# Performance work log

Hardware: AMD Instinct MI355X
Metric: run time of the kernel (lower is better)

Reference implementation:

```python
import jax, jax.numpy as jnp
import numpy as np

ALPHA = 1.0

def setup_inputs() -> dict:
    key = jax.random.key(0)
    k1, k2 = jax.random.split(key)
    x = jax.random.normal(k1, (65536, 512), dtype=jnp.float32)
    clusters = jax.random.normal(k2, (256, 512), dtype=jnp.float32)
    return {"x": x, "clusters": clusters}

def reference(x, clusters):
    # Squared Euclidean distance to each centroid via the GEMM expansion
    x2 = jnp.sum(x * x, axis=1, keepdims=True)            # (B, 1)
    c2 = jnp.sum(clusters * clusters, axis=1)             # (K,)
    cross = x @ clusters.T                                # (B, K) GEMM
    d2 = jnp.maximum(x2 + c2 - 2.0 * cross, 0.0)          # (B, K)
    # Student-t kernel (DEC soft assignment)
    q = 1.0 / (1.0 + d2 / ALPHA)
    q = q ** ((ALPHA + 1.0) / 2.0)
    q = q / jnp.sum(q, axis=1, keepdims=True)             # row-normalize
    return q
```

## Files before the change

### kernel.cpp

```cpp
#include <hip/hip_runtime.h>
#include <hip/hip_bf16.h>


typedef __attribute__((ext_vector_type(4))) short short4v;
typedef __attribute__((ext_vector_type(8))) short short8v;
typedef __attribute__((ext_vector_type(4))) float f32x4;

#define DDIM 512
#define KCL  256
#define BM   64
#define NT   512
#define NTILES 16
#define BTILE  8192

__device__ __forceinline__ short f2bf(float f) {
    __hip_bfloat16 h = __float2bfloat16(f);
    return __builtin_bit_cast(short, h);
}

__device__ __forceinline__ void glds16(const void* g, void* l) {
    __builtin_amdgcn_global_load_lds(
        (const __attribute__((address_space(1))) unsigned int*)g,
        (__attribute__((address_space(3))) unsigned int*)l, 16, 0, 0);
}

__global__ void prep(const float* __restrict__ cl, short* __restrict__ wsB,
                     float* __restrict__ wsC2) {
    const int t = threadIdx.x;
    if (blockIdx.x < 64) {
        const int u = blockIdx.x * 256 + t;
        const int img = u >> 10, gi = u & 1023;
        const int g = gi >> 6, lq = (gi >> 4) & 3, l15 = gi & 15;
        const float* src = cl + (size_t)(g * 16 + l15) * DDIM + img * 32 + lq * 8;
        float4 a = *(const float4*)src;
        float4 b = *(const float4*)(src + 4);
        short8v s;
        s[0]=f2bf(a.x); s[1]=f2bf(a.y); s[2]=f2bf(a.z); s[3]=f2bf(a.w);
        s[4]=f2bf(b.x); s[5]=f2bf(b.y); s[6]=f2bf(b.z); s[7]=f2bf(b.w);
        *(short8v*)&wsB[(size_t)u * 8] = s;
    } else {
        const int cidx = (blockIdx.x - 64) * 16 + (t >> 4);
        const int j = t & 15;
        const float* src = cl + (size_t)cidx * DDIM + j * 32;
        float s = 0.f;
#pragma unroll
        for (int i = 0; i < 8; ++i) {
            float4 v = ((const float4*)src)[i];
            s += v.x*v.x + v.y*v.y + v.z*v.z + v.w*v.w;
        }
        s += __shfl_xor(s, 1); s += __shfl_xor(s, 2);
        s += __shfl_xor(s, 4); s += __shfl_xor(s, 8);
        if (j == 0) wsC2[cidx] = s;
    }
}

#define SFENCE() __builtin_amdgcn_sched_barrier(0)
#define BARV1() asm volatile("s_waitcnt vmcnt(1) lgkmcnt(0)\ns_barrier" ::: "memory")
#define BARV0() asm volatile("s_waitcnt vmcnt(0) lgkmcnt(0)\ns_barrier" ::: "memory")
#define BARV2() asm volatile("s_waitcnt vmcnt(2) lgkmcnt(0)\ns_barrier" ::: "memory")

__global__ __launch_bounds__(NT, 4)
void dec_main(const float* __restrict__ x, const short* __restrict__ wsB,
              const float* __restrict__ wsC2, float* __restrict__ out) {
    __shared__ __align__(16) short lA[2][2048];
    __shared__ __align__(16) short lB[2][8192];
    __shared__ float s_x2[BM];
    __shared__ float s_rs[4][BM];

    const int t = threadIdx.x, lane = t & 63, w = t >> 6;
    const int rg = w >> 2, cg = w & 3;
    const int l15 = lane & 15, lq = lane >> 4;
    const int row0 = blockIdx.x * BM;

    const int srow = t >> 3;
    const int sk4  = (t & 7) << 2;
    const float* xs = x + (size_t)(row0 + srow) * DDIM + sk4;
    const int awr = (srow >> 4) * 512 + (srow & 15) * 32
                  + ((t & 7) >> 1) * 8 + ((t & 7) & 1) * 4;

    f32x4 acc[2][4];
#pragma unroll
    for (int m = 0; m < 2; ++m)
#pragma unroll
        for (int n = 0; n < 4; ++n) acc[m][n] = (f32x4){0.f,0.f,0.f,0.f};
    float x2p = 0.f;
    float4 X0, X1, X2;

#define GLDS(TT, LBN)                                        \
    {  const short* src_ = wsB + (size_t)(TT) * BTILE;       \
       glds16(src_ + t * 8,        (LBN) + t * 8);           \
       glds16(src_ + 4096 + t * 8, (LBN) + 4096 + t * 8); }

#define LOADX(TT, XR)  { XR = *(const float4*)(xs + (TT) * 32); }

#define CVT(XR, LAN)                                                             \
    {  short4v s_;                                                               \
       s_[0]=f2bf(XR.x); s_[1]=f2bf(XR.y); s_[2]=f2bf(XR.z); s_[3]=f2bf(XR.w);   \
       x2p += XR.x*XR.x + XR.y*XR.y + XR.z*XR.z + XR.w*XR.w;                     \
       *(short4v*)&(LAN)[awr] = s_; }

#define MSTEP(LAN, LBN)                                                          \
    {  short8v a0 = *(const short8v*)&(LAN)[rg*1024 + l15*32 + lq*8];            \
       short8v a1 = *(const short8v*)&(LAN)[rg*1024 + 512 + l15*32 + lq*8];      \
       short8v b0 = *(const short8v*)&(LBN)[cg*2048 + lane*8];                   \
       short8v b1 = *(const short8v*)&(LBN)[cg*2048 + 512  + lane*8];            \
       short8v b2 = *(const short8v*)&(LBN)[cg*2048 + 1024 + lane*8];            \
       short8v b3 = *(const short8v*)&(LBN)[cg*2048 + 1536 + lane*8];            \
       acc[0][0] = __builtin_amdgcn_mfma_f32_16x16x32_bf16(a0, b0, acc[0][0], 0,0,0); \
       acc[0][1] = __builtin_amdgcn_mfma_f32_16x16x32_bf16(a0, b1, acc[0][1], 0,0,0); \
       acc[0][2] = __builtin_amdgcn_mfma_f32_16x16x32_bf16(a0, b2, acc[0][2], 0,0,0); \
       acc[0][3] = __builtin_amdgcn_mfma_f32_16x16x32_bf16(a0, b3, acc[0][3], 0,0,0); \
       acc[1][0] = __builtin_amdgcn_mfma_f32_16x16x32_bf16(a1, b0, acc[1][0], 0,0,0); \
       acc[1][1] = __builtin_amdgcn_mfma_f32_16x16x32_bf16(a1, b1, acc[1][1], 0,0,0); \
       acc[1][2] = __builtin_amdgcn_mfma_f32_16x16x32_bf16(a1, b2, acc[1][2], 0,0,0); \
       acc[1][3] = __builtin_amdgcn_mfma_f32_16x16x32_bf16(a1, b3, acc[1][3], 0,0,0); }

#define ITER(J, AC, BC, AN, BN, XC, XL)                                          \
    {  if ((J) + 1 < NTILES) GLDS((J) + 1, BN);                                  \
       SFENCE();                                                                 \
       if ((J) + 1 < NTILES) CVT(XC, AN);                                        \
       MSTEP(AC, BC);                                                            \
       SFENCE();                                                                 \
       if ((J) + 3 < NTILES) { LOADX((J) + 3, XL); }                             \
       SFENCE();                                                                 \
       if ((J) + 1 < NTILES) { if ((J) + 3 < NTILES) BARV1(); else BARV0(); } }

    LOADX(0, X0);
    GLDS(0, lB[0]);
    LOADX(1, X1);
    LOADX(2, X2);
    SFENCE();
    CVT(X0, lA[0]);
    SFENCE();
    BARV2();

    ITER( 0, lA[0], lB[0], lA[1], lB[1], X1, X0)
    ITER( 1, lA[1], lB[1], lA[0], lB[0], X2, X1)
    ITER( 2, lA[0], lB[0], lA[1], lB[1], X0, X2)
    ITER( 3, lA[1], lB[1], lA[0], lB[0], X1, X0)
    ITER( 4, lA[0], lB[0], lA[1], lB[1], X2, X1)
    ITER( 5, lA[1], lB[1], lA[0], lB[0], X0, X2)
    ITER( 6, lA[0], lB[0], lA[1], lB[1], X1, X0)
    ITER( 7, lA[1], lB[1], lA[0], lB[0], X2, X1)
    ITER( 8, lA[0], lB[0], lA[1], lB[1], X0, X2)
    ITER( 9, lA[1], lB[1], lA[0], lB[0], X1, X0)
    ITER(10, lA[0], lB[0], lA[1], lB[1], X2, X1)
    ITER(11, lA[1], lB[1], lA[0], lB[0], X0, X2)
    ITER(12, lA[0], lB[0], lA[1], lB[1], X1, X0)
    ITER(13, lA[1], lB[1], lA[0], lB[0], X2, X1)
    ITER(14, lA[0], lB[0], lA[1], lB[1], X0, X0)
    ITER(15, lA[1], lB[1], lA[0], lB[0], X0, X0)

    x2p += __shfl_xor(x2p, 1); x2p += __shfl_xor(x2p, 2); x2p += __shfl_xor(x2p, 4);
    if ((t & 7) == 0) s_x2[srow] = x2p;
    __syncthreads();

    float c2a[4];
#pragma unroll
    for (int n = 0; n < 4; ++n) c2a[n] = wsC2[cg*64 + n*16 + l15];

#pragma unroll
    for (int m = 0; m < 2; ++m)
#pragma unroll
        for (int n = 0; n < 4; ++n)
#pragma unroll
            for (int r = 0; r < 4; ++r) {
                const int rw = rg*32 + m*16 + lq*4 + r;
                float d2 = fmaxf(s_x2[rw] + c2a[n] - 2.0f * acc[m][n][r], 0.0f);
                acc[m][n][r] = 1.0f / (1.0f + d2);
            }

#pragma unroll
    for (int m = 0; m < 2; ++m)
#pragma unroll
        for (int r = 0; r < 4; ++r) {
            float p = acc[m][0][r] + acc[m][1][r] + acc[m][2][r] + acc[m][3][r];
            p += __shfl_xor(p, 1); p += __shfl_xor(p, 2);
            p += __shfl_xor(p, 4); p += __shfl_xor(p, 8);
            if (l15 == 0) s_rs[cg][rg*32 + m*16 + lq*4 + r] = p;
        }
    __syncthreads();

#pragma unroll
    for (int m = 0; m < 2; ++m)
#pragma unroll
        for (int r = 0; r < 4; ++r) {
            const int rw = rg*32 + m*16 + lq*4 + r;
            const float rinv = 1.0f / (s_rs[0][rw] + s_rs[1][rw] + s_rs[2][rw] + s_rs[3][rw]);
            float* o = out + (size_t)(row0 + rw) * KCL + cg*64 + l15;
#pragma unroll
            for (int n = 0; n < 4; ++n)
                o[n * 16] = acc[m][n][r] * rinv;
        }
}

extern "C" void kernel_launch(void* const* d_in, const int* in_sizes, int n_in,
                              void* d_out, int out_size, void* d_ws, size_t ws_size,
                              hipStream_t stream) {
    const float* x  = (const float*)d_in[0];
    const float* cl = (const float*)d_in[1];
    float* out = (float*)d_out;
    short* wsB  = (short*)d_ws;
    float* wsC2 = (float*)((char*)d_ws + (size_t)NTILES * BTILE * sizeof(short));

    prep<<<80, 256, 0, stream>>>(cl, wsB, wsC2);
    const int B = in_sizes[0] / DDIM;
    dec_main<<<B / BM, NT, 0, stream>>>(x, wsB, wsC2, out);
}
```

Before: 54.07 us.

## Triple-buffer B tiles, single-buffer A with two barriers, raise occupancy

Restructures the K-loop pipeline so centroid tiles sit in a three-slot LDS ring with a prefetch distance of two, while the converted x tile uses one LDS buffer. Each iteration now has two barriers: one after the MFMA reads and one after the next A tile is written. The A layout is rearranged so each lane reads a contiguous 16-byte chunk, the epilogue scratch arrays are aliased onto the A buffer, and launch bounds rise from 4 to 6 blocks per CU. The aim is deeper B prefetch and higher occupancy, at the cost of an extra barrier per iteration and more register pressure.

```diff
diff --git a/kernel.cpp b/kernel.cpp
--- a/kernel.cpp
+++ b/kernel.cpp
@@ -54,18 +54,18 @@
     }
 }
 
-#define SFENCE() __builtin_amdgcn_sched_barrier(0)
-#define BARV1() asm volatile("s_waitcnt vmcnt(1) lgkmcnt(0)\ns_barrier" ::: "memory")
-#define BARV0() asm volatile("s_waitcnt vmcnt(0) lgkmcnt(0)\ns_barrier" ::: "memory")
-#define BARV2() asm volatile("s_waitcnt vmcnt(2) lgkmcnt(0)\ns_barrier" ::: "memory")
-
-__global__ __launch_bounds__(NT, 4)
+#define SFENCE()  __builtin_amdgcn_sched_barrier(0)
+#define BARLGKM() asm volatile("s_waitcnt lgkmcnt(0)\ns_barrier" ::: "memory")
+#define BARV3()   asm volatile("s_waitcnt vmcnt(3) lgkmcnt(0)\ns_barrier" ::: "memory")
+#define BARV0()   asm volatile("s_waitcnt vmcnt(0) lgkmcnt(0)\ns_barrier" ::: "memory")
+
+__global__ __launch_bounds__(NT, 6)
 void dec_main(const float* __restrict__ x, const short* __restrict__ wsB,
               const float* __restrict__ wsC2, float* __restrict__ out) {
-    __shared__ __align__(16) short lA[2][2048];
-    __shared__ __align__(16) short lB[2][8192];
-    __shared__ float s_x2[BM];
-    __shared__ float s_rs[4][BM];
+    __shared__ __align__(16) short lB3[3][BTILE];
+    __shared__ __align__(16) short lA[2048];
+    float* const s_x2 = (float*)lA;
+    float* const s_rs = ((float*)lA) + 64;
 
     const int t = threadIdx.x, lane = t & 63, w = t >> 6;
     const int rg = w >> 2, cg = w & 3;
@@ -73,10 +73,9 @@
     const int row0 = blockIdx.x * BM;
 
     const int srow = t >> 3;
-    const int sk4  = (t & 7) << 2;
-    const float* xs = x + (size_t)(row0 + srow) * DDIM + sk4;
-    const int awr = (srow >> 4) * 512 + (srow & 15) * 32
-                  + ((t & 7) >> 1) * 8 + ((t & 7) & 1) * 4;
+    const float* xs = x + (size_t)(row0 + srow) * DDIM + (t & 7) * 4;
+    const int awr = (srow >> 4) * 512 + ((srow & 15) + 16 * ((t & 7) >> 1)) * 8
+                  + ((t & 7) & 1) * 4;
 
     f32x4 acc[2][4];
 #pragma unroll
@@ -84,7 +83,7 @@
 #pragma unroll
         for (int n = 0; n < 4; ++n) acc[m][n] = (f32x4){0.f,0.f,0.f,0.f};
     float x2p = 0.f;
-    float4 X0, X1, X2;
+    float4 Xa, Xb;
 
 #define GLDS(TT, LBN)                                        \
     {  const short* src_ = wsB + (size_t)(TT) * BTILE;       \
@@ -93,15 +92,15 @@
 
 #define LOADX(TT, XR)  { XR = *(const float4*)(xs + (TT) * 32); }
 
-#define CVT(XR, LAN)                                                             \
+#define CVT(XR)                                                                  \
     {  short4v s_;                                                               \
        s_[0]=f2bf(XR.x); s_[1]=f2bf(XR.y); s_[2]=f2bf(XR.z); s_[3]=f2bf(XR.w);   \
        x2p += XR.x*XR.x + XR.y*XR.y + XR.z*XR.z + XR.w*XR.w;                     \
-       *(short4v*)&(LAN)[awr] = s_; }
-
-#define MSTEP(LAN, LBN)                                                          \
-    {  short8v a0 = *(const short8v*)&(LAN)[rg*1024 + l15*32 + lq*8];            \
-       short8v a1 = *(const short8v*)&(LAN)[rg*1024 + 512 + l15*32 + lq*8];      \
+       *(short4v*)&lA[awr] = s_; }
+
+#define MSTEP(LBN)                                                               \
+    {  short8v a0 = *(const short8v*)&lA[rg*1024 + lane*8];                      \
+       short8v a1 = *(const short8v*)&lA[rg*1024 + 512 + lane*8];                \
        short8v b0 = *(const short8v*)&(LBN)[cg*2048 + lane*8];                   \
        short8v b1 = *(const short8v*)&(LBN)[cg*2048 + 512  + lane*8];            \
        short8v b2 = *(const short8v*)&(LBN)[cg*2048 + 1024 + lane*8];            \
@@ -115,41 +114,46 @@
        acc[1][2] = __builtin_amdgcn_mfma_f32_16x16x32_bf16(a1, b2, acc[1][2], 0,0,0); \
        acc[1][3] = __builtin_amdgcn_mfma_f32_16x16x32_bf16(a1, b3, acc[1][3], 0,0,0); }
 
-#define ITER(J, AC, BC, AN, BN, XC, XL)                                          \
-    {  if ((J) + 1 < NTILES) GLDS((J) + 1, BN);                                  \
+#define ITER(J, BCUR, BNXT, XCON, XLD)                                           \
+    {  if ((J) + 2 < NTILES) { LOADX((J) + 2, XLD); }                            \
        SFENCE();                                                                 \
-       if ((J) + 1 < NTILES) CVT(XC, AN);                                        \
-       MSTEP(AC, BC);                                                            \
+       if ((J) + 2 < NTILES) { GLDS((J) + 2, BNXT); }                            \
        SFENCE();                                                                 \
-       if ((J) + 3 < NTILES) { LOADX((J) + 3, XL); }                             \
+       MSTEP(BCUR);                                                              \
+       BARLGKM();                                                                \
        SFENCE();                                                                 \
-       if ((J) + 1 < NTILES) { if ((J) + 3 < NTILES) BARV1(); else BARV0(); } }
-
-    LOADX(0, X0);
-    GLDS(0, lB[0]);
-    LOADX(1, X1);
-    LOADX(2, X2);
+       if ((J) + 1 < NTILES) {                                                   \
+           CVT(XCON);                                                            \
+           SFENCE();                                                             \
+           if ((J) + 2 < NTILES) BARV3(); else BARV0();                          \
+           SFENCE();                                                             \
+       } }
+
+    LOADX(0, Xa);  SFENCE();
+    GLDS(0, &lB3[0][0]);  SFENCE();
+    LOADX(1, Xb);  SFENCE();
+    GLDS(1, &lB3[1][0]);  SFENCE();
+    CVT(Xa);
     SFENCE();
-    CVT(X0, lA[0]);
+    BARV3();
     SFENCE();
-    BARV2();
-
-    ITER( 0, lA[0], lB[0], lA[1], lB[1], X1, X0)
-    ITER( 1, lA[1], lB[1], lA[0], lB[0], X2, X1)
-    ITER( 2, lA[0], lB[0], lA[1], lB[1], X0, X2)
-    ITER( 3, lA[1], lB[1], lA[0], lB[0], X1, X0)
-    ITER( 4, lA[0], lB[0], lA[1], lB[1], X2, X1)
-    ITER( 5, lA[1], lB[1], lA[0], lB[0], X0, X2)
-    ITER( 6, lA[0], lB[0], lA[1], lB[1], X1, X0)
-    ITER( 7, lA[1], lB[1], lA[0], lB[0], X2, X1)
-    ITER( 8, lA[0], lB[0], lA[1], lB[1], X0, X2)
-    ITER( 9, lA[1], lB[1], lA[0], lB[0], X1, X0)
-    ITER(10, lA[0], lB[0], lA[1], lB[1], X2, X1)
-    ITER(11, lA[1], lB[1], lA[0], lB[0], X0, X2)
-    ITER(12, lA[0], lB[0], lA[1], lB[1], X1, X0)
-    ITER(13, lA[1], lB[1], lA[0], lB[0], X2, X1)
-    ITER(14, lA[0], lB[0], lA[1], lB[1], X0, X0)
-    ITER(15, lA[1], lB[1], lA[0], lB[0], X0, X0)
+
+    ITER( 0, &lB3[0][0], &lB3[2][0], Xb, Xa)
+    ITER( 1, &lB3[1][0], &lB3[0][0], Xa, Xb)
+    ITER( 2, &lB3[2][0], &lB3[1][0], Xb, Xa)
+    ITER( 3, &lB3[0][0], &lB3[2][0], Xa, Xb)
+    ITER( 4, &lB3[1][0], &lB3[0][0], Xb, Xa)
+    ITER( 5, &lB3[2][0], &lB3[1][0], Xa, Xb)
+    ITER( 6, &lB3[0][0], &lB3[2][0], Xb, Xa)
+    ITER( 7, &lB3[1][0], &lB3[0][0], Xa, Xb)
+    ITER( 8, &lB3[2][0], &lB3[1][0], Xb, Xa)
+    ITER( 9, &lB3[0][0], &lB3[2][0], Xa, Xb)
+    ITER(10, &lB3[1][0], &lB3[0][0], Xb, Xa)
+    ITER(11, &lB3[2][0], &lB3[1][0], Xa, Xb)
+    ITER(12, &lB3[0][0], &lB3[2][0], Xb, Xa)
+    ITER(13, &lB3[1][0], &lB3[0][0], Xa, Xb)
+    ITER(14, &lB3[2][0], &lB3[1][0], Xb, Xa)
+    ITER(15, &lB3[0][0], &lB3[2][0], Xa, Xb)
 
     x2p += __shfl_xor(x2p, 1); x2p += __shfl_xor(x2p, 2); x2p += __shfl_xor(x2p, 4);
     if ((t & 7) == 0) s_x2[srow] = x2p;
@@ -177,7 +181,7 @@
             float p = acc[m][0][r] + acc[m][1][r] + acc[m][2][r] + acc[m][3][r];
             p += __shfl_xor(p, 1); p += __shfl_xor(p, 2);
             p += __shfl_xor(p, 4); p += __shfl_xor(p, 8);
-            if (l15 == 0) s_rs[cg][rg*32 + m*16 + lq*4 + r] = p;
+            if (l15 == 0) s_rs[cg*64 + rg*32 + m*16 + lq*4 + r] = p;
         }
     __syncthreads();
 
@@ -186,7 +190,7 @@
 #pragma unroll
         for (int r = 0; r < 4; ++r) {
             const int rw = rg*32 + m*16 + lq*4 + r;
-            const float rinv = 1.0f / (s_rs[0][rw] + s_rs[1][rw] + s_rs[2][rw] + s_rs[3][rw]);
+            const float rinv = 1.0f / (s_rs[rw] + s_rs[64 + rw] + s_rs[128 + rw] + s_rs[192 + rw]);
             float* o = out + (size_t)(row0 + rw) * KCL + cg*64 + l15;
 #pragma unroll
             for (int n = 0; n < 4; ++n)
```

New measurement: 56.62 us. +4.7%, slower.

## Double row tile to 128, triple-buffer centroid tiles, swizzle A LDS layout

Applied to the files above, without the earlier changes.

Each block now covers 128 rows instead of 64, so each wave runs a 4x4 MFMA accumulator grid and every centroid tile loaded into shared memory is reused across twice as many rows. Centroid tiles are triple-buffered and prefetched two stages ahead, and x is loaded as 8-float chunks per thread. A new XOR swizzle on the A tile is meant to reduce LDS bank conflicts. In exchange the block uses more registers and shared memory (about 64 KB) and the grid has half as many blocks, which can lower occupancy and parallelism.

```diff
diff --git a/kernel.cpp b/kernel.cpp
--- a/kernel.cpp
+++ b/kernel.cpp
@@ -2,13 +2,12 @@
 #include <hip/hip_bf16.h>
 
 
-typedef __attribute__((ext_vector_type(4))) short short4v;
 typedef __attribute__((ext_vector_type(8))) short short8v;
 typedef __attribute__((ext_vector_type(4))) float f32x4;
 
 #define DDIM 512
 #define KCL  256
-#define BM   64
+#define BM   128
 #define NT   512
 #define NTILES 16
 #define BTILE  8192
@@ -55,15 +54,14 @@
 }
 
 #define SFENCE() __builtin_amdgcn_sched_barrier(0)
-#define BARV1() asm volatile("s_waitcnt vmcnt(1) lgkmcnt(0)\ns_barrier" ::: "memory")
-#define BARV0() asm volatile("s_waitcnt vmcnt(0) lgkmcnt(0)\ns_barrier" ::: "memory")
-#define BARV2() asm volatile("s_waitcnt vmcnt(2) lgkmcnt(0)\ns_barrier" ::: "memory")
+#define BARV4()  asm volatile("s_waitcnt vmcnt(4) lgkmcnt(0)\ns_barrier" ::: "memory")
+#define BARV0()  asm volatile("s_waitcnt vmcnt(0) lgkmcnt(0)\ns_barrier" ::: "memory")
 
 __global__ __launch_bounds__(NT, 4)
 void dec_main(const float* __restrict__ x, const short* __restrict__ wsB,
               const float* __restrict__ wsC2, float* __restrict__ out) {
-    __shared__ __align__(16) short lA[2][2048];
-    __shared__ __align__(16) short lB[2][8192];
+    __shared__ __align__(16) short lB3[3][BTILE];
+    __shared__ __align__(16) short lA[2][4096];
     __shared__ float s_x2[BM];
     __shared__ float s_rs[4][BM];
 
@@ -72,36 +70,43 @@
     const int l15 = lane & 15, lq = lane >> 4;
     const int row0 = blockIdx.x * BM;
 
-    const int srow = t >> 3;
-    const int sk4  = (t & 7) << 2;
-    const float* xs = x + (size_t)(row0 + srow) * DDIM + sk4;
-    const int awr = (srow >> 4) * 512 + (srow & 15) * 32
-                  + ((t & 7) >> 1) * 8 + ((t & 7) & 1) * 4;
-
-    f32x4 acc[2][4];
-#pragma unroll
-    for (int m = 0; m < 2; ++m)
+    const int R = t >> 2, q = t & 3;
+    const float* xs = x + (size_t)(row0 + R) * DDIM + q * 8;
+    const int awr = ((R >> 4) * 64 + (((R & 15) ^ (2 * q)) + 16 * q)) * 8;
+    const int aoff = (((l15 ^ (2 * lq)) + 16 * lq)) * 8;
+
+    const short* bb = wsB;
+
+    f32x4 acc[4][4];
+#pragma unroll
+    for (int m = 0; m < 4; ++m)
 #pragma unroll
         for (int n = 0; n < 4; ++n) acc[m][n] = (f32x4){0.f,0.f,0.f,0.f};
     float x2p = 0.f;
-    float4 X0, X1, X2;
+    float4 XA0, XA1, XB0, XB1;
 
 #define GLDS(TT, LBN)                                        \
-    {  const short* src_ = wsB + (size_t)(TT) * BTILE;       \
+    {  const short* src_ = bb + (size_t)(TT) * BTILE;        \
        glds16(src_ + t * 8,        (LBN) + t * 8);           \
        glds16(src_ + 4096 + t * 8, (LBN) + 4096 + t * 8); }
 
-#define LOADX(TT, XR)  { XR = *(const float4*)(xs + (TT) * 32); }
-
-#define CVT(XR, LAN)                                                             \
-    {  short4v s_;                                                               \
-       s_[0]=f2bf(XR.x); s_[1]=f2bf(XR.y); s_[2]=f2bf(XR.z); s_[3]=f2bf(XR.w);   \
-       x2p += XR.x*XR.x + XR.y*XR.y + XR.z*XR.z + XR.w*XR.w;                     \
-       *(short4v*)&(LAN)[awr] = s_; }
-
-#define MSTEP(LAN, LBN)                                                          \
-    {  short8v a0 = *(const short8v*)&(LAN)[rg*1024 + l15*32 + lq*8];            \
-       short8v a1 = *(const short8v*)&(LAN)[rg*1024 + 512 + l15*32 + lq*8];      \
+#define LOADX(TT, X0R, X1R)                                  \
+    {  X0R = *(const float4*)(xs + (TT) * 32);               \
+       X1R = *(const float4*)(xs + (TT) * 32 + 4); }
+
+#define CVT(X0R, X1R, ABN)                                                       \
+    {  short8v s_;                                                               \
+       s_[0]=f2bf(X0R.x); s_[1]=f2bf(X0R.y); s_[2]=f2bf(X0R.z); s_[3]=f2bf(X0R.w);\
+       s_[4]=f2bf(X1R.x); s_[5]=f2bf(X1R.y); s_[6]=f2bf(X1R.z); s_[7]=f2bf(X1R.w);\
+       x2p += X0R.x*X0R.x + X0R.y*X0R.y + X0R.z*X0R.z + X0R.w*X0R.w              \
+            + X1R.x*X1R.x + X1R.y*X1R.y + X1R.z*X1R.z + X1R.w*X1R.w;             \
+       *(short8v*)&lA[ABN][awr] = s_; }
+
+#define MSTEP(ABN, LBN)                                                          \
+    {  short8v a0 = *(const short8v*)&lA[ABN][(rg*4+0)*512 + aoff];              \
+       short8v a1 = *(const short8v*)&lA[ABN][(rg*4+1)*512 + aoff];              \
+       short8v a2 = *(const short8v*)&lA[ABN][(rg*4+2)*512 + aoff];              \
+       short8v a3 = *(const short8v*)&lA[ABN][(rg*4+3)*512 + aoff];              \
        short8v b0 = *(const short8v*)&(LBN)[cg*2048 + lane*8];                   \
        short8v b1 = *(const short8v*)&(LBN)[cg*2048 + 512  + lane*8];            \
        short8v b2 = *(const short8v*)&(LBN)[cg*2048 + 1024 + lane*8];            \
@@ -113,46 +118,56 @@
        acc[1][0] = __builtin_amdgcn_mfma_f32_16x16x32_bf16(a1, b0, acc[1][0], 0,0,0); \
        acc[1][1] = __builtin_amdgcn_mfma_f32_16x16x32_bf16(a1, b1, acc[1][1], 0,0,0); \
        acc[1][2] = __builtin_amdgcn_mfma_f32_16x16x32_bf16(a1, b2, acc[1][2], 0,0,0); \
-       acc[1][3] = __builtin_amdgcn_mfma_f32_16x16x32_bf16(a1, b3, acc[1][3], 0,0,0); }
-
-#define ITER(J, AC, BC, AN, BN, XC, XL)                                          \
-    {  if ((J) + 1 < NTILES) GLDS((J) + 1, BN);                                  \
+       acc[1][3] = __builtin_amdgcn_mfma_f32_16x16x32_bf16(a1, b3, acc[1][3], 0,0,0); \
+       acc[2][0] = __builtin_amdgcn_mfma_f32_16x16x32_bf16(a2, b0, acc[2][0], 0,0,0); \
+       acc[2][1] = __builtin_amdgcn_mfma_f32_16x16x32_bf16(a2, b1, acc[2][1], 0,0,0); \
+       acc[2][2] = __builtin_amdgcn_mfma_f32_16x16x32_bf16(a2, b2, acc[2][2], 0,0,0); \
+       acc[2][3] = __builtin_amdgcn_mfma_f32_16x16x32_bf16(a2, b3, acc[2][3], 0,0,0); \
+       acc[3][0] = __builtin_amdgcn_mfma_f32_16x16x32_bf16(a3, b0, acc[3][0], 0,0,0); \
+       acc[3][1] = __builtin_amdgcn_mfma_f32_16x16x32_bf16(a3, b1, acc[3][1], 0,0,0); \
+       acc[3][2] = __builtin_amdgcn_mfma_f32_16x16x32_bf16(a3, b2, acc[3][2], 0,0,0); \
+       acc[3][3] = __builtin_amdgcn_mfma_f32_16x16x32_bf16(a3, b3, acc[3][3], 0,0,0); }
+
+#define ITER(J, ABC, ABN, BCUR, BNXT, XC0, XC1, XL0, XL1)                        \
+    {  if ((J) + 2 < NTILES) { LOADX((J) + 2, XL0, XL1); }                       \
        SFENCE();                                                                 \
-       if ((J) + 1 < NTILES) CVT(XC, AN);                                        \
-       MSTEP(AC, BC);                                                            \
+       if ((J) + 2 < NTILES) { GLDS((J) + 2, BNXT); }                            \
        SFENCE();                                                                 \
-       if ((J) + 3 < NTILES) { LOADX((J) + 3, XL); }                             \
+       if ((J) + 1 < NTILES) { CVT(XC0, XC1, ABN); }                             \
+       MSTEP(ABC, BCUR);                                                         \
        SFENCE();                                                                 \
-       if ((J) + 1 < NTILES) { if ((J) + 3 < NTILES) BARV1(); else BARV0(); } }
-
-    LOADX(0, X0);
-    GLDS(0, lB[0]);
-    LOADX(1, X1);
-    LOADX(2, X2);
+       if ((J) + 2 < NTILES) { BARV4(); }                                        \
+       else if ((J) + 1 < NTILES) { BARV0(); }                                   \
+       SFENCE(); }
+
+    LOADX(0, XA0, XA1);  SFENCE();
+    GLDS(0, &lB3[0][0]); SFENCE();
+    LOADX(1, XB0, XB1);  SFENCE();
+    GLDS(1, &lB3[1][0]); SFENCE();
+    CVT(XA0, XA1, 0);
     SFENCE();
-    CVT(X0, lA[0]);
+    BARV4();
     SFENCE();
-    BARV2();
-
-    ITER( 0, lA[0], lB[0], lA[1], lB[1], X1, X0)
-    ITER( 1, lA[1], lB[1], lA[0], lB[0], X2, X1)
-    ITER( 2, lA[0], lB[0], lA[1], lB[1], X0, X2)
-    ITER( 3, lA[1], lB[1], lA[0], lB[0], X1, X0)
-    ITER( 4, lA[0], lB[0], lA[1], lB[1], X2, X1)
-    ITER( 5, lA[1], lB[1], lA[0], lB[0], X0, X2)
-    ITER( 6, lA[0], lB[0], lA[1], lB[1], X1, X0)
-    ITER( 7, lA[1], lB[1], lA[0], lB[0], X2, X1)
-    ITER( 8, lA[0], lB[0], lA[1], lB[1], X0, X2)
-    ITER( 9, lA[1], lB[1], lA[0], lB[0], X1, X0)
-    ITER(10, lA[0], lB[0], lA[1], lB[1], X2, X1)
-    ITER(11, lA[1], lB[1], lA[0], lB[0], X0, X2)
-    ITER(12, lA[0], lB[0], lA[1], lB[1], X1, X0)
-    ITER(13, lA[1], lB[1], lA[0], lB[0], X2, X1)
-    ITER(14, lA[0], lB[0], lA[1], lB[1], X0, X0)
-    ITER(15, lA[1], lB[1], lA[0], lB[0], X0, X0)
-
-    x2p += __shfl_xor(x2p, 1); x2p += __shfl_xor(x2p, 2); x2p += __shfl_xor(x2p, 4);
-    if ((t & 7) == 0) s_x2[srow] = x2p;
+
+    ITER( 0, 0, 1, &lB3[0][0], &lB3[2][0], XB0, XB1, XA0, XA1)
+    ITER( 1, 1, 0, &lB3[1][0], &lB3[0][0], XA0, XA1, XB0, XB1)
+    ITER( 2, 0, 1, &lB3[2][0], &lB3[1][0], XB0, XB1, XA0, XA1)
+    ITER( 3, 1, 0, &lB3[0][0], &lB3[2][0], XA0, XA1, XB0, XB1)
+    ITER( 4, 0, 1, &lB3[1][0], &lB3[0][0], XB0, XB1, XA0, XA1)
+    ITER( 5, 1, 0, &lB3[2][0], &lB3[1][0], XA0, XA1, XB0, XB1)
+    ITER( 6, 0, 1, &lB3[0][0], &lB3[2][0], XB0, XB1, XA0, XA1)
+    ITER( 7, 1, 0, &lB3[1][0], &lB3[0][0], XA0, XA1, XB0, XB1)
+    ITER( 8, 0, 1, &lB3[2][0], &lB3[1][0], XB0, XB1, XA0, XA1)
+    ITER( 9, 1, 0, &lB3[0][0], &lB3[2][0], XA0, XA1, XB0, XB1)
+    ITER(10, 0, 1, &lB3[1][0], &lB3[0][0], XB0, XB1, XA0, XA1)
+    ITER(11, 1, 0, &lB3[2][0], &lB3[1][0], XA0, XA1, XB0, XB1)
+    ITER(12, 0, 1, &lB3[0][0], &lB3[2][0], XB0, XB1, XA0, XA1)
+    ITER(13, 1, 0, &lB3[1][0], &lB3[0][0], XA0, XA1, XB0, XB1)
+    ITER(14, 0, 1, &lB3[2][0], &lB3[1][0], XB0, XB1, XA0, XA1)
+    ITER(15, 1, 0, &lB3[0][0], &lB3[2][0], XA0, XA1, XB0, XB1)
+
+    x2p += __shfl_xor(x2p, 1); x2p += __shfl_xor(x2p, 2);
+    if (q == 0) s_x2[R] = x2p;
     __syncthreads();
 
     float c2a[4];
@@ -160,32 +175,32 @@
     for (int n = 0; n < 4; ++n) c2a[n] = wsC2[cg*64 + n*16 + l15];
 
 #pragma unroll
-    for (int m = 0; m < 2; ++m)
+    for (int m = 0; m < 4; ++m)
 #pragma unroll
         for (int n = 0; n < 4; ++n)
 #pragma unroll
             for (int r = 0; r < 4; ++r) {
-                const int rw = rg*32 + m*16 + lq*4 + r;
+                const int rw = rg*64 + m*16 + lq*4 + r;
                 float d2 = fmaxf(s_x2[rw] + c2a[n] - 2.0f * acc[m][n][r], 0.0f);
                 acc[m][n][r] = 1.0f / (1.0f + d2);
             }
 
 #pragma unroll
-    for (int m = 0; m < 2; ++m)
+    for (int m = 0; m < 4; ++m)
 #pragma unroll
         for (int r = 0; r < 4; ++r) {
             float p = acc[m][0][r] + acc[m][1][r] + acc[m][2][r] + acc[m][3][r];
             p += __shfl_xor(p, 1); p += __shfl_xor(p, 2);
             p += __shfl_xor(p, 4); p += __shfl_xor(p, 8);
-            if (l15 == 0) s_rs[cg][rg*32 + m*16 + lq*4 + r] = p;
+            if (l15 == 0) s_rs[cg][rg*64 + m*16 + lq*4 + r] = p;
         }
     __syncthreads();
 
 #pragma unroll
-    for (int m = 0; m < 2; ++m)
+    for (int m = 0; m < 4; ++m)
 #pragma unroll
         for (int r = 0; r < 4; ++r) {
-            const int rw = rg*32 + m*16 + lq*4 + r;
+            const int rw = rg*64 + m*16 + lq*4 + r;
             const float rinv = 1.0f / (s_rs[0][rw] + s_rs[1][rw] + s_rs[2][rw] + s_rs[3][rw]);
             float* o = out + (size_t)(row0 + rw) * KCL + cg*64 + l15;
 #pragma unroll
```

After: 49.18 us, median of 2. -9.0%, faster.
